# Kernel tuning notes

Measured on AMD Instinct MI355X. Metric: run time of the kernel, lower is better.

## Reference

```python
import jax, jax.numpy as jnp
import numpy as np

N_NODES = 100000
N_EDGES = 1600000
IN_DIM = 256
HIDDEN = 128


def setup_inputs() -> dict:
    key = jax.random.key(0)
    ks = jax.random.split(key, 8)
    x = jax.random.normal(ks[0], (N_NODES, IN_DIM), dtype=jnp.float32)
    edge_index = jax.random.randint(ks[1], (2, N_EDGES), 0, N_NODES, dtype=jnp.int64)
    W0 = jax.random.normal(ks[2], (IN_DIM, HIDDEN), dtype=jnp.float32) / np.sqrt(IN_DIM)
    b0 = jnp.zeros((HIDDEN,), dtype=jnp.float32)
    Wmu = jax.random.normal(ks[3], (HIDDEN, HIDDEN), dtype=jnp.float32) / np.sqrt(HIDDEN)
    bmu = jnp.zeros((HIDDEN,), dtype=jnp.float32)
    Wsig = jax.random.normal(ks[4], (HIDDEN, HIDDEN), dtype=jnp.float32) / np.sqrt(HIDDEN)
    bsig = jnp.zeros((HIDDEN,), dtype=jnp.float32)
    return {"x": x, "edge_index": edge_index, "W0": W0, "b0": b0,
            "Wmu": Wmu, "bmu": bmu, "Wsig": Wsig, "bsig": bsig}


def reference(x, edge_index, W0, b0, Wmu, bmu, Wsig, bsig):
    N = x.shape[0]
    # PyG gcn_norm: add self-loops (weight 1), deg over target (col),
    # norm = deg^-1/2[row] * w * deg^-1/2[col]
    loops = jnp.arange(N, dtype=edge_index.dtype)
    row = jnp.concatenate([edge_index[0], loops])  # sources
    col = jnp.concatenate([edge_index[1], loops])  # targets
    w = jnp.ones(row.shape[0], dtype=x.dtype)
    deg = jax.ops.segment_sum(w, col, num_segments=N)
    dinv = jnp.where(deg > 0, jax.lax.rsqrt(deg), 0.0).astype(x.dtype)
    norm = dinv[row] * dinv[col]  # [E+N]

    def gcn_conv(h, W, b):
        h = h @ W                                   # dense transform [N, out]
        msg = norm[:, None] * h[row]                # gather + scale [E+N, out]
        return jax.ops.segment_sum(msg, col, num_segments=N) + b

    h = jax.nn.relu(gcn_conv(x, W0, b0))
    mu = gcn_conv(h, Wmu, bmu)
    sigma = jax.nn.softplus(gcn_conv(h, Wsig, bsig)) + 1e-7
    return mu, sigma
```

## Files before the change

### kernel.cpp

```cpp
#include <hip/hip_runtime.h>
#include <math.h>

#define N_NODES 100000
#define N_EDGES 1600000
#define ROWB    512
#define HALFB   51200000ull
#define NBKT    196
#define BSH     9
#define BCAP    10240
#define EPB     1024

typedef float  f32x4  __attribute__((ext_vector_type(4)));
typedef __bf16 bf16x8 __attribute__((ext_vector_type(8)));
typedef short  s16x8  __attribute__((ext_vector_type(8)));
typedef unsigned long long u64;

__device__ __forceinline__ unsigned short f2bf(float f) {
    unsigned int u = __builtin_bit_cast(unsigned int, f);
    u += 0x7FFFu + ((u >> 16) & 1u);
    return (unsigned short)(u >> 16);
}
__device__ __forceinline__ float bf2f(unsigned short h) {
    unsigned int u = ((unsigned int)h) << 16;
    return __builtin_bit_cast(float, u);
}
__device__ __forceinline__ float bf_lo(unsigned int u) {
    return __builtin_bit_cast(float, u << 16);
}
__device__ __forceinline__ float bf_hi(unsigned int u) {
    return __builtin_bit_cast(float, u & 0xFFFF0000u);
}
__device__ __forceinline__ bf16x8 packhi(const float4& a, const float4& b) {
    float v[8] = {a.x, a.y, a.z, a.w, b.x, b.y, b.z, b.w};
    s16x8 hh;
    #pragma unroll
    for (int j = 0; j < 8; j++) hh[j] = (short)f2bf(v[j]);
    return __builtin_bit_cast(bf16x8, hh);
}
__device__ __forceinline__ void ntstore4(void* p, f32x4 v) {
    __builtin_nontemporal_store(v, (f32x4*)p);
}
__device__ __forceinline__ float fast_sp(float x) {
    return fmaxf(x, 0.f) + __logf(1.f + __expf(-fabsf(x))) + 1e-7f;
}

#define MFMA16(a, b, c) __builtin_amdgcn_mfma_f32_16x16x32_bf16((a), (b), (c), 0, 0, 0)


__launch_bounds__(256)
__global__ void bin_kernel(const int* __restrict__ row, const int* __restrict__ col,
                           int* __restrict__ gcur, u64* __restrict__ entries) {
    __shared__ int hist[NBKT], base[NBKT], cur[NBKT];
    const int tid = threadIdx.x;
    for (int i = tid; i < NBKT; i += 256) { hist[i] = 0; cur[i] = 0; }
    __syncthreads();
    const int e0 = blockIdx.x * EPB;
    int cols[4];
    #pragma unroll
    for (int it = 0; it < 4; it++) {
        int e = e0 + it * 256 + tid;
        int c = (e < N_EDGES) ? col[e] : -1;
        cols[it] = c;
        if (c >= 0) atomicAdd(&hist[c >> BSH], 1);
    }
    __syncthreads();
    for (int i = tid; i < NBKT; i += 256)
        base[i] = atomicAdd(&gcur[i], hist[i]);
    __syncthreads();
    #pragma unroll
    for (int it = 0; it < 4; it++) {
        int e = e0 + it * 256 + tid;
        int c = cols[it];
        if (c >= 0) {
            int b = c >> BSH;
            int r = atomicAdd(&cur[b], 1);
            entries[(size_t)b * BCAP + base[b] + r] =
                ((u64)(unsigned)c << 32) | (unsigned)row[e];
        }
    }
}


__global__ void bktscan_kernel(const int* __restrict__ gcur, int* __restrict__ bktBase) {
    __shared__ int s[256];
    const int tid = threadIdx.x;
    int v = (tid < NBKT) ? gcur[tid] : 0;
    s[tid] = v;
    __syncthreads();
    for (int d = 1; d < 256; d <<= 1) {
        int t = (tid >= d) ? s[tid - d] : 0;
        __syncthreads();
        s[tid] += t;
        __syncthreads();
    }
    if (tid < NBKT) bktBase[tid] = s[tid] - v;
}


__launch_bounds__(256)
__global__ void csr_kernel(const u64* __restrict__ entries, const int* __restrict__ gcur,
                           const int* __restrict__ bktBase,
                           int* __restrict__ cnt, int* __restrict__ offs,
                           float* __restrict__ dinv, int* __restrict__ sortedRow) {
    __shared__ int lcnt[512], sA[512], sB[512], lcur[512];
    const int b = blockIdx.x, tid = threadIdx.x;
    const int n0 = b << BSH;
    lcnt[tid] = 0; lcnt[tid + 256] = 0;
    __syncthreads();
    const int nb = gcur[b], base = bktBase[b];
    const u64* ep = entries + (size_t)b * BCAP;
    for (int i = tid; i < nb; i += 256)
        atomicAdd(&lcnt[(int)(ep[i] >> 32) - n0], 1);
    __syncthreads();
    sA[tid] = lcnt[tid]; sA[tid + 256] = lcnt[tid + 256];
    __syncthreads();
    int* src = sA; int* dst = sB;
    for (int d = 1; d < 512; d <<= 1) {
        #pragma unroll
        for (int k = tid; k < 512; k += 256)
            dst[k] = src[k] + ((k >= d) ? src[k - d] : 0);
        __syncthreads();
        int* t = src; src = dst; dst = t;
    }
    #pragma unroll
    for (int k = tid; k < 512; k += 256) {
        int excl = src[k] - lcnt[k];
        lcur[k] = excl;
        int node = n0 + k;
        if (node < N_NODES) {
            offs[node] = base + excl;
            cnt[node]  = lcnt[k];
            dinv[node] = rsqrtf((float)(lcnt[k] + 1));
        }
    }
    __syncthreads();
    for (int i = tid; i < nb; i += 256) {
        u64 pk = ep[i];
        int local = (int)(pk >> 32) - n0;
        int p = base + atomicAdd(&lcur[local], 1);
        sortedRow[p] = (int)(pk & 0xFFFFFFFFu);
    }
}


__global__ void prep_w(const float* __restrict__ W0, const float* __restrict__ Wmu,
                       const float* __restrict__ Wsig,
                       unsigned short* __restrict__ W0h, unsigned short* __restrict__ W0l,
                       unsigned short* __restrict__ Wmsh, unsigned short* __restrict__ Wmsl) {
    int c = blockIdx.x;
    int k = threadIdx.x;
    if (c < 128) {
        float v = W0[k * 128 + c];
        unsigned short h = f2bf(v);
        W0h[c * 256 + k] = h;
        W0l[c * 256 + k] = f2bf(v - bf2f(h));
    } else if (k < 128) {
        int c2 = c - 128;
        float v = (c2 < 128) ? Wmu[k * 128 + c2] : Wsig[k * 128 + (c2 - 128)];
        unsigned short h = f2bf(v);
        Wmsh[c2 * 128 + k] = h;
        Wmsl[c2 * 128 + k] = f2bf(v - bf2f(h));
    }
}


__launch_bounds__(256, 3)
__global__ void gemm1_mfma(const float* __restrict__ x,
                           const unsigned short* __restrict__ Wh,
                           const unsigned short* __restrict__ Wl,
                           char* __restrict__ t0base, int t0stride) {
    __shared__ __align__(16) char L[49152];
    const int tid = threadIdx.x;
    const int wave = tid >> 6, lane = tid & 63;
    const int lrow = lane & 15, q4 = lane >> 4;
    const int swz = (lrow & 7) << 4;
    const int n0 = blockIdx.x * 64;

    bf16x8 b[8];
    {
        int node = n0 + wave * 16 + lrow;
        int nc = node > N_NODES - 1 ? N_NODES - 1 : node;
        const float* xp = x + (size_t)nc * 256 + q4 * 8;
        #pragma unroll
        for (int ks = 0; ks < 8; ks++) {
            float4 p0 = *(const float4*)(xp + ks * 32);
            float4 p1 = *(const float4*)(xp + ks * 32 + 4);
            b[ks] = packhi(p0, p1);
        }
    }

    int sgo[4], slo[4];
    #pragma unroll
    for (int j = 0; j < 4; j++) {
        int u = tid + 256 * j;
        int col = (u >> 5) & 15, k8 = (u & 31) * 8;
        sgo[j] = col * 256 + k8;
        slo[j] = (j >= 2 ? 8192 : 0) + ((col * 512 + k8 * 2) ^ ((col & 7) << 4));
    }

    {
        int4 sw[4];
        #pragma unroll
        for (int j = 0; j < 4; j++)
            sw[j] = *(const int4*)((j >= 2 ? Wl : Wh) + sgo[j]);
        #pragma unroll
        for (int j = 0; j < 4; j++)
            *(int4*)(L + slo[j]) = sw[j];
    }
    __syncthreads();

    #pragma unroll
    for (int ct = 0; ct < 8; ct++) {
        int4 sw[4];
        if (ct < 7) {
            #pragma unroll
            for (int j = 0; j < 4; j++)
                sw[j] = *(const int4*)((j >= 2 ? Wl : Wh) + (ct + 1) * 16 * 256 + sgo[j]);
        }
        const char* bufp = L + (ct & 1) * 16384;
        f32x4 acc = {};
        #pragma unroll
        for (int hl = 0; hl < 2; hl++) {
            bf16x8 w[8];
            #pragma unroll
            for (int ks = 0; ks < 8; ks++)
                w[ks] = *(const bf16x8*)(bufp + hl * 8192 +
                        ((lrow * 512 + ks * 64 + q4 * 16) ^ swz));
            #pragma unroll
            for (int ks = 0; ks < 8; ks++)
                acc = MFMA16(w[ks], b[ks], acc);
        }
        {
            int node_l = wave * 16 + lrow;
            int a = (node_l * 256 + ct * 32 + q4 * 8) ^ ((node_l & 7) << 4);
            ushort4 p = make_ushort4(f2bf(acc[0]), f2bf(acc[1]),
                                     f2bf(acc[2]), f2bf(acc[3]));
            *(ushort4*)(L + 32768 + a) = p;
        }
        if (ct < 7) {
            #pragma unroll
            for (int j = 0; j < 4; j++)
                *(int4*)(L + (((ct + 1) & 1) * 16384) + slo[j]) = sw[j];
            __syncthreads();
        }
    }
    __syncthreads();
    #pragma unroll
    for (int it = 0; it < 4; it++) {
        int linear = it * 4096 + tid * 16;
        int node_l = linear >> 8, off = linear & 255;
        int4 v = *(const int4*)(L + 32768 + (linear ^ ((node_l & 7) << 4)));
        int node = n0 + node_l;
        if (node < N_NODES)
            *(int4*)(t0base + (size_t)node * t0stride + off) = v;
    }
}


template <int EPI>
__launch_bounds__(256)
__global__ void agg_bf16(const char* __restrict__ srcBase, char* __restrict__ dstBase,
                         int stride,
                         const int* __restrict__ offs, const int* __restrict__ cnt,
                         const int* __restrict__ sortedRow, const float* __restrict__ dinv,
                         const float* __restrict__ bias) {
    const int n = blockIdx.x * 4 + (threadIdx.x >> 6);
    const int lane = threadIdx.x & 63;
    const int laneB = lane * 4;
    const float dn = dinv[n];
    unsigned int u = *(const unsigned int*)(srcBase + (size_t)n * stride + laneB);
    const float ws = dn * dn;
    float acc0 = ws * bf_lo(u);
    float acc1 = ws * bf_hi(u);
    const int start = __builtin_amdgcn_readfirstlane(offs[n]);
    const int num   = __builtin_amdgcn_readfirstlane(cnt[n]);

    int i = 0;
    for (; i + 8 <= num; i += 8) {
        int myr = sortedRow[start + i + (lane & 7)];
        int rs[8];
        #pragma unroll
        for (int j = 0; j < 8; j++) rs[j] = __builtin_amdgcn_readlane(myr, j);
        unsigned int ue[8];
        #pragma unroll
        for (int j = 0; j < 8; j++) {
            const char* p = srcBase + (size_t)rs[j] * stride;
            ue[j] = *(const unsigned int*)(p + laneB);
        }
        float w[8];
        #pragma unroll
        for (int j = 0; j < 8; j++) w[j] = dn * dinv[rs[j]];
        #pragma unroll
        for (int j = 0; j < 8; j++) {
            acc0 = fmaf(w[j], bf_lo(ue[j]), acc0);
            acc1 = fmaf(w[j], bf_hi(ue[j]), acc1);
        }
    }
    for (; i < num; i++) {
        int rsv = __builtin_amdgcn_readfirstlane(sortedRow[start + i]);
        const char* p = srcBase + (size_t)rsv * stride;
        unsigned int ue = *(const unsigned int*)(p + laneB);
        float w = dn * dinv[rsv];
        acc0 = fmaf(w, bf_lo(ue), acc0);
        acc1 = fmaf(w, bf_hi(ue), acc1);
    }

    if (EPI) {
        acc0 = fmaxf(acc0 + bias[2 * lane], 0.f);
        acc1 = fmaxf(acc1 + bias[2 * lane + 1], 0.f);
    }
    unsigned int o = (unsigned int)f2bf(acc0) | ((unsigned int)f2bf(acc1) << 16);
    *(unsigned int*)(dstBase + (size_t)n * stride + laneB) = o;
}


__launch_bounds__(256, 4)
__global__ void gemm2_mfma(const unsigned short* __restrict__ Wh,
                           const unsigned short* __restrict__ Wl,
                           const float* __restrict__ bmu, const float* __restrict__ bsig,
                           const char* __restrict__ t2base, int t2stride,
                           char* __restrict__ outc) {
    __shared__ __align__(16) char L[16384];
    const int tid = threadIdx.x;
    const int wave = tid >> 6, lane = tid & 63;
    const int lrow = lane & 15, q4 = lane >> 4;
    const int swz = (lrow & 7) << 4;
    const int n0 = blockIdx.x * 64;

    const int node = n0 + wave * 16 + lrow;
    const bool ok = node < N_NODES;
    bf16x8 b[4];
    {
        int nc = node > N_NODES - 1 ? N_NODES - 1 : node;
        const char* ap = t2base + (size_t)nc * t2stride + q4 * 16;
        #pragma unroll
        for (int ki = 0; ki < 4; ki++)
            b[ki] = *(const bf16x8*)(ap + ki * 64);
    }

    const int colS = tid >> 4, k8S = (tid & 15) * 8;
    const int sgo = colS * 128 + k8S;
    const int sloc = (colS * 256 + k8S * 2) ^ ((colS & 7) << 4);

    {
        int4 h = *(const int4*)(Wh + sgo);
        int4 l = *(const int4*)(Wl + sgo);
        *(int4*)(L + sloc) = h;
        *(int4*)(L + 4096 + sloc) = l;
    }
    __syncthreads();

    #pragma unroll
    for (int ct = 0; ct < 16; ct++) {
        int4 swh, swl;
        if (ct < 15) {
            swh = *(const int4*)(Wh + (ct + 1) * 2048 + sgo);
            swl = *(const int4*)(Wl + (ct + 1) * 2048 + sgo);
        }
        const char* bufp = L + (ct & 1) * 8192;
        f32x4 acc = {};
        #pragma unroll
        for (int hl = 0; hl < 2; hl++) {
            bf16x8 w[4];
            #pragma unroll
            for (int ki = 0; ki < 4; ki++)
                w[ki] = *(const bf16x8*)(bufp + hl * 4096 +
                        ((lrow * 256 + ki * 64 + q4 * 16) ^ swz));
            #pragma unroll
            for (int ki = 0; ki < 4; ki++)
                acc = MFMA16(w[ki], b[ki], acc);
        }
        const int f0 = (ct & 7) * 16 + q4 * 4;
        if (ct < 8) {
            if (ok) {
                float4 bv = *(const float4*)(bmu + f0);
                f32x4 o = {acc[0] + bv.x, acc[1] + bv.y, acc[2] + bv.z, acc[3] + bv.w};
                ntstore4(outc + (size_t)node * ROWB + f0 * 4, o);
            }
        } else {
            if (ok) {
                float4 bv = *(const float4*)(bsig + f0);
                f32x4 o;
                #pragma unroll
                for (int q = 0; q < 4; q++)
                    o[q] = fast_sp(acc[q] + ((const float*)&bv)[q]);
                ntstore4(outc + HALFB + (size_t)node * ROWB + f0 * 4, o);
            }
        }
        if (ct < 15) {
            char* nb = L + ((ct + 1) & 1) * 8192;
            *(int4*)(nb + sloc) = swh;
            *(int4*)(nb + 4096 + sloc) = swl;
            __syncthreads();
        }
    }
}


extern "C" void kernel_launch(void* const* d_in, const int* in_sizes, int n_in,
                              void* d_out, int out_size, void* d_ws, size_t ws_size,
                              hipStream_t stream) {
    const float* x    = (const float*)d_in[0];
    const int*   ei   = (const int*)d_in[1];
    const int*   row  = ei;
    const int*   col  = ei + N_EDGES;
    const float* W0   = (const float*)d_in[2];
    const float* b0   = (const float*)d_in[3];
    const float* Wmu  = (const float*)d_in[4];
    const float* bmu  = (const float*)d_in[5];
    const float* Wsig = (const float*)d_in[6];
    const float* bsig = (const float*)d_in[7];
    char* outc = (char*)d_out;
    char* wsb  = (char*)d_ws;

    size_t o = 0;
    auto take = [&](size_t nbytes) {
        size_t r = o; o += (nbytes + 255) & ~(size_t)255; return r;
    };
    size_t oW0h = take(65536), oW0l = take(65536);
    size_t oWmsh = take(65536), oWmsl = take(65536);
    size_t oGcur = take(NBKT * 4), oBkt = take(NBKT * 4);
    size_t oCnt = take(N_NODES * 4), oOffs = take(N_NODES * 4), oDinv = take(N_NODES * 4);
    size_t oSort = take(N_EDGES * 4);
    size_t oEnt = take((size_t)NBKT * BCAP * 8);
    size_t oT0 = take((size_t)N_NODES * 256);
    size_t oH  = take((size_t)N_NODES * 256);
    const bool dense = (ws_size >= o);

    unsigned short* W0h  = (unsigned short*)(wsb + oW0h);
    unsigned short* W0l  = (unsigned short*)(wsb + oW0l);
    unsigned short* Wmsh = (unsigned short*)(wsb + oWmsh);
    unsigned short* Wmsl = (unsigned short*)(wsb + oWmsl);
    int*   gcur      = (int*)(wsb + oGcur);
    int*   bktBase   = (int*)(wsb + oBkt);
    int*   cnt       = (int*)(wsb + oCnt);
    int*   offs      = (int*)(wsb + oOffs);
    float* dinvp     = (float*)(wsb + oDinv);
    int*   sortedRow = (int*)(wsb + oSort);

    u64* entries; char *t0b, *hb, *t2b; int stride;
    if (dense) {
        entries = (u64*)(wsb + oEnt);
        t0b = wsb + oT0;  hb = wsb + oH;  t2b = wsb + oT0;
        stride = 256;
    } else {
        entries = (u64*)(outc + HALFB);
        t0b = outc + 256; hb = outc + HALFB; t2b = outc;
        stride = ROWB;
    }

    hipMemsetAsync(gcur, 0, NBKT * sizeof(int), stream);
    prep_w<<<384, 256, 0, stream>>>(W0, Wmu, Wsig, W0h, W0l, Wmsh, Wmsl);
    bin_kernel<<<(N_EDGES + EPB - 1) / EPB, 256, 0, stream>>>(row, col, gcur, entries);
    bktscan_kernel<<<1, 256, 0, stream>>>(gcur, bktBase);
    csr_kernel<<<NBKT, 256, 0, stream>>>(entries, gcur, bktBase, cnt, offs, dinvp, sortedRow);

    gemm1_mfma<<<(N_NODES + 63) / 64, 256, 0, stream>>>(x, W0h, W0l, t0b, stride);
    agg_bf16<1><<<N_NODES / 4, 256, 0, stream>>>(t0b, hb, stride,
                                                 offs, cnt, sortedRow, dinvp, b0);
    agg_bf16<0><<<N_NODES / 4, 256, 0, stream>>>(hb, t2b, stride,
                                                 offs, cnt, sortedRow, dinvp, nullptr);
    gemm2_mfma<<<(N_NODES + 63) / 64, 256, 0, stream>>>(Wmsh, Wmsl, bmu, bsig,
                                                        t2b, stride, outc);
}
```

Measured before the change: 279.9 us.

## Fuse preprocessing kernels into combined launches and split gemm2 across output halves

Weight prep is merged into the edge-binning kernel. The separate bucket scan is replaced by a per-block reduction inside the CSR build, which is fused with gemm1 as extra blocks in one launch. This cuts kernel launches and the serial scan step. The workspace layout gains a middle tier so the second aggregation writes into a dedicated buffer, which lets gemm2 split mu and sigma into two block halves for more parallelism, at the cost of reloading the activations in each half. CSR blocks and gemm1 blocks run concurrently without dependencies, and each CSR block redundantly sums up to 196 counters.

```diff
diff --git a/kernel.cpp b/kernel.cpp
--- a/kernel.cpp
+++ b/kernel.cpp
@@ -9,6 +9,7 @@
 #define BSH     9
 #define BCAP    10240
 #define EPB     1024
+#define PREPB   384
 
 typedef float  f32x4  __attribute__((ext_vector_type(4)));
 typedef __bf16 bf16x8 __attribute__((ext_vector_type(8)));
@@ -48,13 +49,34 @@
 
 
 __launch_bounds__(256)
-__global__ void bin_kernel(const int* __restrict__ row, const int* __restrict__ col,
-                           int* __restrict__ gcur, u64* __restrict__ entries) {
+__global__ void k1_prep_bin(const float* __restrict__ W0, const float* __restrict__ Wmu,
+                            const float* __restrict__ Wsig,
+                            unsigned short* __restrict__ W0h, unsigned short* __restrict__ W0l,
+                            unsigned short* __restrict__ Wmsh, unsigned short* __restrict__ Wmsl,
+                            const int* __restrict__ row, const int* __restrict__ col,
+                            int* __restrict__ gcur, u64* __restrict__ entries) {
     __shared__ int hist[NBKT], base[NBKT], cur[NBKT];
     const int tid = threadIdx.x;
+    if (blockIdx.x < PREPB) {
+        int c = blockIdx.x, k = tid;
+        if (c < 128) {
+            float v = W0[k * 128 + c];
+            unsigned short h = f2bf(v);
+            W0h[c * 256 + k] = h;
+            W0l[c * 256 + k] = f2bf(v - bf2f(h));
+        } else if (k < 128) {
+            int c2 = c - 128;
+            float v = (c2 < 128) ? Wmu[k * 128 + c2] : Wsig[k * 128 + (c2 - 128)];
+            unsigned short h = f2bf(v);
+            Wmsh[c2 * 128 + k] = h;
+            Wmsl[c2 * 128 + k] = f2bf(v - bf2f(h));
+        }
+        return;
+    }
+    const int bid = blockIdx.x - PREPB;
     for (int i = tid; i < NBKT; i += 256) { hist[i] = 0; cur[i] = 0; }
     __syncthreads();
-    const int e0 = blockIdx.x * EPB;
+    const int e0 = bid * EPB;
     int cols[4];
     #pragma unroll
     for (int it = 0; it < 4; it++) {
@@ -81,100 +103,74 @@
 }
 
 
-__global__ void bktscan_kernel(const int* __restrict__ gcur, int* __restrict__ bktBase) {
-    __shared__ int s[256];
-    const int tid = threadIdx.x;
-    int v = (tid < NBKT) ? gcur[tid] : 0;
-    s[tid] = v;
-    __syncthreads();
-    for (int d = 1; d < 256; d <<= 1) {
-        int t = (tid >= d) ? s[tid - d] : 0;
-        __syncthreads();
-        s[tid] += t;
-        __syncthreads();
-    }
-    if (tid < NBKT) bktBase[tid] = s[tid] - v;
-}
-
-
-__launch_bounds__(256)
-__global__ void csr_kernel(const u64* __restrict__ entries, const int* __restrict__ gcur,
-                           const int* __restrict__ bktBase,
-                           int* __restrict__ cnt, int* __restrict__ offs,
-                           float* __restrict__ dinv, int* __restrict__ sortedRow) {
-    __shared__ int lcnt[512], sA[512], sB[512], lcur[512];
-    const int b = blockIdx.x, tid = threadIdx.x;
-    const int n0 = b << BSH;
-    lcnt[tid] = 0; lcnt[tid + 256] = 0;
-    __syncthreads();
-    const int nb = gcur[b], base = bktBase[b];
-    const u64* ep = entries + (size_t)b * BCAP;
-    for (int i = tid; i < nb; i += 256)
-        atomicAdd(&lcnt[(int)(ep[i] >> 32) - n0], 1);
-    __syncthreads();
-    sA[tid] = lcnt[tid]; sA[tid + 256] = lcnt[tid + 256];
-    __syncthreads();
-    int* src = sA; int* dst = sB;
-    for (int d = 1; d < 512; d <<= 1) {
-        #pragma unroll
-        for (int k = tid; k < 512; k += 256)
-            dst[k] = src[k] + ((k >= d) ? src[k - d] : 0);
-        __syncthreads();
-        int* t = src; src = dst; dst = t;
-    }
-    #pragma unroll
-    for (int k = tid; k < 512; k += 256) {
-        int excl = src[k] - lcnt[k];
-        lcur[k] = excl;
-        int node = n0 + k;
-        if (node < N_NODES) {
-            offs[node] = base + excl;
-            cnt[node]  = lcnt[k];
-            dinv[node] = rsqrtf((float)(lcnt[k] + 1));
-        }
-    }
-    __syncthreads();
-    for (int i = tid; i < nb; i += 256) {
-        u64 pk = ep[i];
-        int local = (int)(pk >> 32) - n0;
-        int p = base + atomicAdd(&lcur[local], 1);
-        sortedRow[p] = (int)(pk & 0xFFFFFFFFu);
-    }
-}
-
-
-__global__ void prep_w(const float* __restrict__ W0, const float* __restrict__ Wmu,
-                       const float* __restrict__ Wsig,
-                       unsigned short* __restrict__ W0h, unsigned short* __restrict__ W0l,
-                       unsigned short* __restrict__ Wmsh, unsigned short* __restrict__ Wmsl) {
-    int c = blockIdx.x;
-    int k = threadIdx.x;
-    if (c < 128) {
-        float v = W0[k * 128 + c];
-        unsigned short h = f2bf(v);
-        W0h[c * 256 + k] = h;
-        W0l[c * 256 + k] = f2bf(v - bf2f(h));
-    } else if (k < 128) {
-        int c2 = c - 128;
-        float v = (c2 < 128) ? Wmu[k * 128 + c2] : Wsig[k * 128 + (c2 - 128)];
-        unsigned short h = f2bf(v);
-        Wmsh[c2 * 128 + k] = h;
-        Wmsl[c2 * 128 + k] = f2bf(v - bf2f(h));
-    }
-}
-
-
 __launch_bounds__(256, 3)
-__global__ void gemm1_mfma(const float* __restrict__ x,
-                           const unsigned short* __restrict__ Wh,
-                           const unsigned short* __restrict__ Wl,
-                           char* __restrict__ t0base, int t0stride) {
+__global__ void k2_csr_gemm1(const u64* __restrict__ entries, const int* __restrict__ gcur,
+                             int* __restrict__ cnt, int* __restrict__ offs,
+                             float* __restrict__ dinv, int* __restrict__ sortedRow,
+                             const float* __restrict__ x,
+                             const unsigned short* __restrict__ Wh,
+                             const unsigned short* __restrict__ Wl,
+                             char* __restrict__ t0base, int t0stride) {
     __shared__ __align__(16) char L[49152];
     const int tid = threadIdx.x;
+
+    if (blockIdx.x < NBKT) {
+        int* lcnt = (int*)L;
+        int* sA   = lcnt + 512;
+        int* sB   = sA + 512;
+        int* lcur = sB + 512;
+        int* red  = lcur + 512;
+        const int b = blockIdx.x, n0 = b << BSH;
+        red[tid] = (tid < b) ? gcur[tid] : 0;
+        __syncthreads();
+        for (int d = 128; d > 0; d >>= 1) {
+            if (tid < d) red[tid] += red[tid + d];
+            __syncthreads();
+        }
+        const int base = red[0];
+        const int nb = gcur[b];
+        lcnt[tid] = 0; lcnt[tid + 256] = 0;
+        __syncthreads();
+        const u64* ep = entries + (size_t)b * BCAP;
+        for (int i = tid; i < nb; i += 256)
+            atomicAdd(&lcnt[(int)(ep[i] >> 32) - n0], 1);
+        __syncthreads();
+        sA[tid] = lcnt[tid]; sA[tid + 256] = lcnt[tid + 256];
+        __syncthreads();
+        int* src = sA; int* dst = sB;
+        for (int d = 1; d < 512; d <<= 1) {
+            #pragma unroll
+            for (int k = tid; k < 512; k += 256)
+                dst[k] = src[k] + ((k >= d) ? src[k - d] : 0);
+            __syncthreads();
+            int* t = src; src = dst; dst = t;
+        }
+        #pragma unroll
+        for (int k = tid; k < 512; k += 256) {
+            int excl = src[k] - lcnt[k];
+            lcur[k] = excl;
+            int node = n0 + k;
+            if (node < N_NODES) {
+                offs[node] = base + excl;
+                cnt[node]  = lcnt[k];
+                dinv[node] = rsqrtf((float)(lcnt[k] + 1));
+            }
+        }
+        __syncthreads();
+        for (int i = tid; i < nb; i += 256) {
+            u64 pk = ep[i];
+            int local = (int)(pk >> 32) - n0;
+            int p = base + atomicAdd(&lcur[local], 1);
+            sortedRow[p] = (int)(pk & 0xFFFFFFFFu);
+        }
+        return;
+    }
+
+    const int bid = blockIdx.x - NBKT;
     const int wave = tid >> 6, lane = tid & 63;
     const int lrow = lane & 15, q4 = lane >> 4;
     const int swz = (lrow & 7) << 4;
-    const int n0 = blockIdx.x * 64;
+    const int n0 = bid * 64;
 
     bf16x8 b[8];
     {
@@ -260,7 +256,7 @@
 template <int EPI>
 __launch_bounds__(256)
 __global__ void agg_bf16(const char* __restrict__ srcBase, char* __restrict__ dstBase,
-                         int stride,
+                         int srcStride, int dstStride,
                          const int* __restrict__ offs, const int* __restrict__ cnt,
                          const int* __restrict__ sortedRow, const float* __restrict__ dinv,
                          const float* __restrict__ bias) {
@@ -268,7 +264,7 @@
     const int lane = threadIdx.x & 63;
     const int laneB = lane * 4;
     const float dn = dinv[n];
-    unsigned int u = *(const unsigned int*)(srcBase + (size_t)n * stride + laneB);
+    unsigned int u = *(const unsigned int*)(srcBase + (size_t)n * srcStride + laneB);
     const float ws = dn * dn;
     float acc0 = ws * bf_lo(u);
     float acc1 = ws * bf_hi(u);
@@ -284,7 +280,7 @@
         unsigned int ue[8];
         #pragma unroll
         for (int j = 0; j < 8; j++) {
-            const char* p = srcBase + (size_t)rs[j] * stride;
+            const char* p = srcBase + (size_t)rs[j] * srcStride;
             ue[j] = *(const unsigned int*)(p + laneB);
         }
         float w[8];
@@ -298,7 +294,7 @@
     }
     for (; i < num; i++) {
         int rsv = __builtin_amdgcn_readfirstlane(sortedRow[start + i]);
-        const char* p = srcBase + (size_t)rsv * stride;
+        const char* p = srcBase + (size_t)rsv * srcStride;
         unsigned int ue = *(const unsigned int*)(p + laneB);
         float w = dn * dinv[rsv];
         acc0 = fmaf(w, bf_lo(ue), acc0);
@@ -310,10 +306,11 @@
         acc1 = fmaxf(acc1 + bias[2 * lane + 1], 0.f);
     }
     unsigned int o = (unsigned int)f2bf(acc0) | ((unsigned int)f2bf(acc1) << 16);
-    *(unsigned int*)(dstBase + (size_t)n * stride + laneB) = o;
-}
-
-
+    *(unsigned int*)(dstBase + (size_t)n * dstStride + laneB) = o;
+}
+
+
+template <int SPLIT>
 __launch_bounds__(256, 4)
 __global__ void gemm2_mfma(const unsigned short* __restrict__ Wh,
                            const unsigned short* __restrict__ Wl,
@@ -325,7 +322,10 @@
     const int wave = tid >> 6, lane = tid & 63;
     const int lrow = lane & 15, q4 = lane >> 4;
     const int swz = (lrow & 7) << 4;
-    const int n0 = blockIdx.x * 64;
+    const int half = SPLIT ? (blockIdx.x & 1) : 0;
+    const int nb2  = SPLIT ? (blockIdx.x >> 1) : blockIdx.x;
+    const int n0 = nb2 * 64;
+    const int CT = SPLIT ? 8 : 16;
 
     const int node = n0 + wave * 16 + lrow;
     const bool ok = node < N_NODES;
@@ -341,21 +341,22 @@
     const int colS = tid >> 4, k8S = (tid & 15) * 8;
     const int sgo = colS * 128 + k8S;
     const int sloc = (colS * 256 + k8S * 2) ^ ((colS & 7) << 4);
+    const int g0 = half * 8;
 
     {
-        int4 h = *(const int4*)(Wh + sgo);
-        int4 l = *(const int4*)(Wl + sgo);
+        int4 h = *(const int4*)(Wh + g0 * 2048 + sgo);
+        int4 l = *(const int4*)(Wl + g0 * 2048 + sgo);
         *(int4*)(L + sloc) = h;
         *(int4*)(L + 4096 + sloc) = l;
     }
     __syncthreads();
 
-    #pragma unroll
-    for (int ct = 0; ct < 16; ct++) {
+    for (int ct = 0; ct < CT; ct++) {
+        const int gct = g0 + ct;
         int4 swh, swl;
-        if (ct < 15) {
-            swh = *(const int4*)(Wh + (ct + 1) * 2048 + sgo);
-            swl = *(const int4*)(Wl + (ct + 1) * 2048 + sgo);
+        if (ct < CT - 1) {
+            swh = *(const int4*)(Wh + (gct + 1) * 2048 + sgo);
+            swl = *(const int4*)(Wl + (gct + 1) * 2048 + sgo);
         }
         const char* bufp = L + (ct & 1) * 8192;
         f32x4 acc = {};
@@ -370,8 +371,8 @@
             for (int ki = 0; ki < 4; ki++)
                 acc = MFMA16(w[ki], b[ki], acc);
         }
-        const int f0 = (ct & 7) * 16 + q4 * 4;
-        if (ct < 8) {
+        const int f0 = (gct & 7) * 16 + q4 * 4;
+        if (gct < 8) {
             if (ok) {
                 float4 bv = *(const float4*)(bmu + f0);
                 f32x4 o = {acc[0] + bv.x, acc[1] + bv.y, acc[2] + bv.z, acc[3] + bv.w};
@@ -387,7 +388,7 @@
                 ntstore4(outc + HALFB + (size_t)node * ROWB + f0 * 4, o);
             }
         }
-        if (ct < 15) {
+        if (ct < CT - 1) {
             char* nb = L + ((ct + 1) & 1) * 8192;
             *(int4*)(nb + sloc) = swh;
             *(int4*)(nb + 4096 + sloc) = swl;
@@ -419,47 +420,47 @@
     };
     size_t oW0h = take(65536), oW0l = take(65536);
     size_t oWmsh = take(65536), oWmsl = take(65536);
-    size_t oGcur = take(NBKT * 4), oBkt = take(NBKT * 4);
+    size_t oGcur = take(NBKT * 4);
     size_t oCnt = take(N_NODES * 4), oOffs = take(N_NODES * 4), oDinv = take(N_NODES * 4);
     size_t oSort = take(N_EDGES * 4);
+    size_t oT2 = take((size_t)N_NODES * 256);  size_t endT2 = o;
     size_t oEnt = take((size_t)NBKT * BCAP * 8);
     size_t oT0 = take((size_t)N_NODES * 256);
-    size_t oH  = take((size_t)N_NODES * 256);
-    const bool dense = (ws_size >= o);
+    size_t oH  = take((size_t)N_NODES * 256);  size_t endAll = o;
+    const int tier = (ws_size >= endAll) ? 2 : (ws_size >= endT2 ? 1 : 0);
 
     unsigned short* W0h  = (unsigned short*)(wsb + oW0h);
     unsigned short* W0l  = (unsigned short*)(wsb + oW0l);
     unsigned short* Wmsh = (unsigned short*)(wsb + oWmsh);
     unsigned short* Wmsl = (unsigned short*)(wsb + oWmsl);
     int*   gcur      = (int*)(wsb + oGcur);
-    int*   bktBase   = (int*)(wsb + oBkt);
     int*   cnt       = (int*)(wsb + oCnt);
     int*   offs      = (int*)(wsb + oOffs);
     float* dinvp     = (float*)(wsb + oDinv);
     int*   sortedRow = (int*)(wsb + oSort);
 
-    u64* entries; char *t0b, *hb, *t2b; int stride;
-    if (dense) {
-        entries = (u64*)(wsb + oEnt);
-        t0b = wsb + oT0;  hb = wsb + oH;  t2b = wsb + oT0;
-        stride = 256;
-    } else {
-        entries = (u64*)(outc + HALFB);
-        t0b = outc + 256; hb = outc + HALFB; t2b = outc;
-        stride = ROWB;
-    }
+    u64* entries = (tier == 2) ? (u64*)(wsb + oEnt) : (u64*)(outc + HALFB);
+    char* t0b; int sT0;
+    char* hb;  int sH;
+    char* t2b; int sT2;
+    if (tier == 2) { t0b = wsb + oT0; sT0 = 256; hb = wsb + oH; sH = 256; }
+    else           { t0b = outc + 256; sT0 = ROWB; hb = outc + HALFB; sH = ROWB; }
+    if (tier >= 1) { t2b = wsb + oT2; sT2 = 256; }
+    else           { t2b = outc; sT2 = ROWB; }
 
     hipMemsetAsync(gcur, 0, NBKT * sizeof(int), stream);
-    prep_w<<<384, 256, 0, stream>>>(W0, Wmu, Wsig, W0h, W0l, Wmsh, Wmsl);
-    bin_kernel<<<(N_EDGES + EPB - 1) / EPB, 256, 0, stream>>>(row, col, gcur, entries);
-    bktscan_kernel<<<1, 256, 0, stream>>>(gcur, bktBase);
-    csr_kernel<<<NBKT, 256, 0, stream>>>(entries, gcur, bktBase, cnt, offs, dinvp, sortedRow);
-
-    gemm1_mfma<<<(N_NODES + 63) / 64, 256, 0, stream>>>(x, W0h, W0l, t0b, stride);
-    agg_bf16<1><<<N_NODES / 4, 256, 0, stream>>>(t0b, hb, stride,
+    k1_prep_bin<<<PREPB + (N_EDGES + EPB - 1) / EPB, 256, 0, stream>>>(
+        W0, Wmu, Wsig, W0h, W0l, Wmsh, Wmsl, row, col, gcur, entries);
+    k2_csr_gemm1<<<NBKT + (N_NODES + 63) / 64, 256, 0, stream>>>(
+        entries, gcur, cnt, offs, dinvp, sortedRow, x, W0h, W0l, t0b, sT0);
+    agg_bf16<1><<<N_NODES / 4, 256, 0, stream>>>(t0b, hb, sT0, sH,
                                                  offs, cnt, sortedRow, dinvp, b0);
-    agg_bf16<0><<<N_NODES / 4, 256, 0, stream>>>(hb, t2b, stride,
+    agg_bf16<0><<<N_NODES / 4, 256, 0, stream>>>(hb, t2b, sH, sT2,
                                                  offs, cnt, sortedRow, dinvp, nullptr);
-    gemm2_mfma<<<(N_NODES + 63) / 64, 256, 0, stream>>>(Wmsh, Wmsl, bmu, bsig,
-                                                        t2b, stride, outc);
-}
+    if (tier >= 1)
+        gemm2_mfma<1><<<2 * ((N_NODES + 63) / 64), 256, 0, stream>>>(
+            Wmsh, Wmsl, bmu, bsig, t2b, sT2, outc);
+    else
+        gemm2_mfma<0><<<(N_NODES + 63) / 64, 256, 0, stream>>>(
+            Wmsh, Wmsl, bmu, bsig, t2b, sT2, outc);
+}
```

Measured after the change: 255.7 us. -8.7%, faster.
